# Kernel optimization log

Hardware: AMD Instinct MI355X
Metric: run time of the kernel (lower is better)

The kernel has to match this reference:

```python
import jax, jax.numpy as jnp
import numpy as np

B, L, D = 32, 256, 512
D_STATE, D_CONV, EXPAND, NODE_DIM, D_FF = 16, 4, 2, 16, 2048
D_INNER = EXPAND * D
DT_RANK = D // 16


def _layernorm(x, g, b, eps=1e-5):
    mu = x.mean(-1, keepdims=True)
    var = ((x - mu) ** 2).mean(-1, keepdims=True)
    return (x - mu) * jax.lax.rsqrt(var + eps) * g + b


def _mamba(x, in_w, conv_w, conv_b, xproj_w, dt_w, dt_b, A_log, Dp, out_w):
    # Standard selective-scan (S6) Mamba inner block.
    Bb, Ll, _ = x.shape
    u, z = jnp.split(x @ in_w, 2, axis=-1)                # (B,L,d_inner) each
    pad = jnp.pad(u, ((0, 0), (D_CONV - 1, 0), (0, 0)))   # causal depthwise conv1d
    u = sum(pad[:, k:k + Ll, :] * conv_w[:, k] for k in range(D_CONV)) + conv_b
    u = jax.nn.silu(u)
    proj = u @ xproj_w                                    # (B,L,dt_rank+2*d_state)
    dt, Bm, Cm = jnp.split(proj, [DT_RANK, DT_RANK + D_STATE], axis=-1)
    dt = jax.nn.softplus(dt @ dt_w + dt_b)                # (B,L,d_inner)
    A = -jnp.exp(A_log)                                   # (d_inner,d_state)
    dA = jnp.exp(dt[..., None] * A)                       # (B,L,d_inner,d_state)
    dBu = dt[..., None] * Bm[:, :, None, :] * u[..., None]

    def step(h, inp):
        dA_t, dBu_t, C_t = inp
        h = dA_t * h + dBu_t
        return h, jnp.einsum('bds,bs->bd', h, C_t)

    h0 = jnp.zeros((Bb, D_INNER, D_STATE), x.dtype)
    _, ys = jax.lax.scan(step, h0, (dA.transpose(1, 0, 2, 3),
                                    dBu.transpose(1, 0, 2, 3),
                                    Cm.transpose(1, 0, 2)))
    y = ys.transpose(1, 0, 2) + u * Dp                    # (B,L,d_inner)
    return (y * jax.nn.silu(z)) @ out_w


def _forward(x,
             d_in_w, d_conv_w, d_conv_b, d_xproj_w, d_dt_w, d_dt_b, d_A_log, d_D, d_out_w, d_ln_g, d_ln_b,
             s_emb1, s_emb2, s_in_w, s_conv_w, s_conv_b, s_xproj_w, s_dt_w, s_dt_b, s_A_log, s_D, s_out_w, s_ln_g, s_ln_b,
             f_ln_g, f_ln_b, f_w1, f_b1, f_w2, f_b2):
    # DiffSSM: selective SSM on the first-differenced sequence, residual + LN
    xd = jnp.concatenate([x[:, :1], x[:, 1:] - x[:, :-1]], axis=1)
    x = _layernorm(x + _mamba(xd, d_in_w, d_conv_w, d_conv_b, d_xproj_w,
                              d_dt_w, d_dt_b, d_A_log, d_D, d_out_w),
                   d_ln_g, d_ln_b)
    # SpatialGraphMamba: learned adjacency over enc_in tokens, graph mix, SSM
    adj = jax.nn.softmax(jax.nn.relu(s_emb1 @ s_emb2.T), axis=-1)  # (enc_in,enc_in)
    xg = jnp.einsum('nl,bld->bnd', adj, x)
    x = _layernorm(x + _mamba(xg, s_in_w, s_conv_w, s_conv_b, s_xproj_w,
                              s_dt_w, s_dt_b, s_A_log, s_D, s_out_w),
                   s_ln_g, s_ln_b)
    # Pre-norm FFN with residual
    h = _layernorm(x, f_ln_g, f_ln_b)
    x = x + jax.nn.gelu(h @ f_w1 + f_b1) @ f_w2 + f_b2
    return x, adj


def setup_inputs() -> dict:
    key = jax.random.key(0)
    ks = iter(jax.random.split(key, 64))

    def rn(shape, s=0.02):
        return jax.random.normal(next(ks), shape, jnp.float32) * s

    A_log_init = jnp.log(jnp.broadcast_to(
        jnp.arange(1, D_STATE + 1, dtype=jnp.float32), (D_INNER, D_STATE)))
    dt_b_init = jnp.full((D_INNER,), -4.6, jnp.float32)  # softplus^-1(~0.01)

    inp = {'x': jax.random.normal(next(ks), (B, L, D), jnp.float32)}
    for p in ('d_', 's_'):
        inp[p + 'in_w'] = rn((D, 2 * D_INNER))
        inp[p + 'conv_w'] = rn((D_INNER, D_CONV), 0.1)
        inp[p + 'conv_b'] = jnp.zeros((D_INNER,), jnp.float32)
        inp[p + 'xproj_w'] = rn((D_INNER, DT_RANK + 2 * D_STATE))
        inp[p + 'dt_w'] = rn((DT_RANK, D_INNER))
        inp[p + 'dt_b'] = dt_b_init
        inp[p + 'A_log'] = A_log_init
        inp[p + 'D'] = jnp.ones((D_INNER,), jnp.float32)
        inp[p + 'out_w'] = rn((D_INNER, D))
        inp[p + 'ln_g'] = jnp.ones((D,), jnp.float32)
        inp[p + 'ln_b'] = jnp.zeros((D,), jnp.float32)
    inp['s_emb1'] = rn((L, NODE_DIM), 0.1)
    inp['s_emb2'] = rn((L, NODE_DIM), 0.1)
    inp['f_ln_g'] = jnp.ones((D,), jnp.float32)
    inp['f_ln_b'] = jnp.zeros((D,), jnp.float32)
    inp['f_w1'] = rn((D, D_FF))
    inp['f_b1'] = jnp.zeros((D_FF,), jnp.float32)
    inp['f_w2'] = rn((D_FF, D))
    inp['f_b2'] = jnp.zeros((D,), jnp.float32)
    return inp


def reference(x,
              d_in_w, d_conv_w, d_conv_b, d_xproj_w, d_dt_w, d_dt_b, d_A_log, d_D, d_out_w, d_ln_g, d_ln_b,
              s_emb1, s_emb2, s_in_w, s_conv_w, s_conv_b, s_xproj_w, s_dt_w, s_dt_b, s_A_log, s_D, s_out_w, s_ln_g, s_ln_b,
              f_ln_g, f_ln_b, f_w1, f_b1, f_w2, f_b2):
    return _forward(x,
                    d_in_w, d_conv_w, d_conv_b, d_xproj_w, d_dt_w, d_dt_b, d_A_log, d_D, d_out_w, d_ln_g, d_ln_b,
                    s_emb1, s_emb2, s_in_w, s_conv_w, s_conv_b, s_xproj_w, s_dt_w, s_dt_b, s_A_log, s_D, s_out_w, s_ln_g, s_ln_b,
                    f_ln_g, f_ln_b, f_w1, f_b1, f_w2, f_b2)
```

## Files before the change

kernel.cpp:

```cpp
#include <hip/hip_runtime.h>

#define DEV __device__ __forceinline__

typedef __bf16 bf16x8 __attribute__((ext_vector_type(8)));
typedef float  f32x4  __attribute__((ext_vector_type(4)));

DEV unsigned short f2b(float f) {
    union { float f; unsigned u; } v; v.f = f;
    unsigned r = v.u + 0x7fffu + ((v.u >> 16) & 1u);
    return (unsigned short)(r >> 16);
}
DEV float b2f(unsigned short h) {
    union { unsigned u; float f; } v; v.u = ((unsigned)h) << 16;
    return v.f;
}
DEV float sigmoidf_(float x) { return 1.f / (1.f + __expf(-x)); }
DEV float geluf_(float x) {
    float t = 0.7978845608028654f * (x + 0.044715f * x * x * x);
    return 0.5f * x * (1.f + tanhf(t));
}
DEV float softplusf_(float x) { return x > 15.f ? x : log1pf(__expf(x)); }
DEV void gload_lds16(const void* g, void* l) {
    __builtin_amdgcn_global_load_lds((const __attribute__((address_space(1))) void*)g,
                                     (__attribute__((address_space(3))) void*)l, 16, 0, 0);
}


struct WtDesc { const float* s; unsigned short* d; int K; int N; int t0; };
struct WtArgs { WtDesc m[12]; };

__global__ __launch_bounds__(256) void wtrans_k(WtArgs a) {
    __shared__ float tile[32][33];
    int t = blockIdx.x;
    int mi = 0;
#pragma unroll
    for (int j = 1; j < 12; j++) if (t >= a.m[j].t0) mi = j;
    const float* src0 = a.m[mi].s;
    unsigned short* dst0 = a.m[mi].d;
    const int K = a.m[mi].K, N = a.m[mi].N;
    const int lt = t - a.m[mi].t0;
    const int ntk = K >> 5;
    const int kt = lt % ntk, nt = lt / ntk;
    const int c = threadIdx.x & 31, r = threadIdx.x >> 5;
    const float* src = src0 + (size_t)(kt * 32) * N + nt * 32;
#pragma unroll
    for (int i = 0; i < 4; i++) tile[r + i * 8][c] = src[(size_t)(r + i * 8) * N + c];
    __syncthreads();
    unsigned short* dst = dst0 + (size_t)(nt * 32) * K + kt * 32;
#pragma unroll
    for (int i = 0; i < 4; i++) dst[(size_t)(r + i * 8) * K + c] = f2b(tile[c][r + i * 8]);
}

__global__ __launch_bounds__(256) void diff_k(const float* __restrict__ x,
                                              unsigned short* __restrict__ xd) {
    size_t i4 = (size_t)blockIdx.x * 256 + threadIdx.x;
    size_t idx = i4 * 4;
    int l = (int)((idx >> 9) & 255);
    float4 v = *(const float4*)&x[idx];
    if (l > 0) {
        float4 p = *(const float4*)&x[idx - 512];
        v.x -= p.x; v.y -= p.y; v.z -= p.z; v.w -= p.w;
    }
    unsigned short o[4] = {f2b(v.x), f2b(v.y), f2b(v.z), f2b(v.w)};
    *(unsigned long long*)&xd[idx] = *(unsigned long long*)o;
}

__global__ __launch_bounds__(256) void adj_k(const float* __restrict__ e1,
                                             const float* __restrict__ e2,
                                             float* __restrict__ adjf,
                                             unsigned short* __restrict__ adjb) {
    const int n = blockIdx.x, tid = threadIdx.x;
    __shared__ float e1s[16];
    __shared__ float redm[4], reds[4];
    if (tid < 16) e1s[tid] = e1[n * 16 + tid];
    __syncthreads();
    const float* e2r = e2 + tid * 16;
    float dot = 0.f;
#pragma unroll
    for (int k = 0; k < 16; k++) dot = fmaf(e1s[k], e2r[k], dot);
    float v = fmaxf(dot, 0.f);
    float m = v;
#pragma unroll
    for (int o = 32; o > 0; o >>= 1) m = fmaxf(m, __shfl_xor(m, o));
    const int lane = tid & 63, wv = tid >> 6;
    if (lane == 0) redm[wv] = m;
    __syncthreads();
    m = fmaxf(fmaxf(redm[0], redm[1]), fmaxf(redm[2], redm[3]));
    float e = __expf(v - m);
    float ssum = e;
#pragma unroll
    for (int o = 32; o > 0; o >>= 1) ssum += __shfl_xor(ssum, o);
    if (lane == 0) reds[wv] = ssum;
    __syncthreads();
    ssum = reds[0] + reds[1] + reds[2] + reds[3];
    float o = e / ssum;
    adjf[(size_t)n * 256 + tid] = o;
    adjb[(size_t)n * 256 + tid] = f2b(o);
}

template<int HBIAS, int HGELU>
__global__ __launch_bounds__(512, 2) void gemm256_k(
    const unsigned short* __restrict__ A, const unsigned short* __restrict__ Bt,
    unsigned short* __restrict__ C, const float* __restrict__ bias,
    int M, int N, int K, int lda) {
    constexpr int BM = 256, BN = 256, BK = 64;
    __shared__ __align__(16) unsigned short As[2][BM * BK];
    __shared__ __align__(16) unsigned short Bs[2][BN * BK];
    const int tid  = threadIdx.x;
    const int lane = tid & 63;
    const int wave = tid >> 6;
    const int wr = wave >> 2;
    const int wc = wave & 3;
    const int bm = blockIdx.x * BM, bn = blockIdx.y * BN;
    const int lrow  = lane & 15;
    const int klane = lane >> 4;

    f32x4 acc[8][4];
#pragma unroll
    for (int m = 0; m < 8; m++)
#pragma unroll
        for (int n = 0; n < 4; n++) {
            acc[m][n][0] = 0.f; acc[m][n][1] = 0.f; acc[m][n][2] = 0.f; acc[m][n][3] = 0.f;
        }

    auto STAGE = [&](int buf, int k0) {
#pragma unroll
        for (int it = 0; it < 4; ++it) {
            int flat = (it * 512 + tid) * 8;
            int r = flat >> 6, s = (flat & 63) >> 3;
            int c = (s ^ (r & 7)) * 8;
            gload_lds16(A + (size_t)(bm + r) * lda + (k0 + c),
                        &As[buf][(it * 512 + (tid & 448)) * 8]);
        }
#pragma unroll
        for (int it = 0; it < 4; ++it) {
            int flat = (it * 512 + tid) * 8;
            int r = flat >> 6, s = (flat & 63) >> 3;
            int c = (s ^ (r & 7)) * 8;
            gload_lds16(Bt + (size_t)(bn + r) * K + (k0 + c),
                        &Bs[buf][(it * 512 + (tid & 448)) * 8]);
        }
    };
    auto COMPUTE = [&](int buf) {
#pragma unroll
        for (int kk = 0; kk < 2; kk++) {
            bf16x8 af[8], bfv[4];
#pragma unroll
            for (int m = 0; m < 8; m++) {
                int rr = wr * 128 + m * 16 + lrow;
                int sl = (kk * 4 + klane) ^ (rr & 7);
                af[m] = *(const bf16x8*)&As[buf][rr * BK + sl * 8];
            }
#pragma unroll
            for (int n = 0; n < 4; n++) {
                int rr = wc * 64 + n * 16 + lrow;
                int sl = (kk * 4 + klane) ^ (rr & 7);
                bfv[n] = *(const bf16x8*)&Bs[buf][rr * BK + sl * 8];
            }
#pragma unroll
            for (int m = 0; m < 8; m++)
#pragma unroll
                for (int n = 0; n < 4; n++)
                    acc[m][n] = __builtin_amdgcn_mfma_f32_16x16x32_bf16(af[m], bfv[n], acc[m][n], 0, 0, 0);
        }
    };

    const int nt = K / BK;
    STAGE(0, 0);
    __syncthreads();
    for (int t = 0; t < nt; t += 2) {
        if (t + 1 < nt) STAGE(1, (t + 1) * BK);
        COMPUTE(0);
        __syncthreads();
        if (t + 1 < nt) {
            if (t + 2 < nt) STAGE(0, (t + 2) * BK);
            COMPUTE(1);
            if (t + 2 < nt) __syncthreads();
        }
    }

    const int r0 = (lane >> 4) << 2;
    unsigned short* Cs = As[0];
    constexpr int PITCH = BN + 8;
#pragma unroll
    for (int g = 0; g < 8; g++) {
        __syncthreads();
        if (wr == (g >> 2)) {
#pragma unroll
            for (int mm = 0; mm < 2; mm++) {
                const int m = (g & 3) * 2 + mm;
#pragma unroll
                for (int n = 0; n < 4; n++) {
                    const int cl = wc * 64 + n * 16 + lrow;
                    float bv = HBIAS ? bias[bn + cl] : 0.f;
#pragma unroll
                    for (int j = 0; j < 4; j++) {
                        float v = acc[m][n][j] + bv;
                        if (HGELU) v = geluf_(v);
                        Cs[(mm * 16 + r0 + j) * PITCH + cl] = f2b(v);
                    }
                }
            }
        }
        __syncthreads();
#pragma unroll
        for (int i = 0; i < 2; i++) {
            int flat = (i * 512 + tid) * 8;
            int row = flat >> 8, col = flat & 255;
            uint4 val = *(const uint4*)&Cs[row * PITCH + col];
            *(uint4*)&C[(size_t)(bm + g * 32 + row) * N + bn + col] = val;
        }
    }
}

template<int BM, int BN, int BK, int WRN, int FM, int FN,
         int OBF, int HBIAS, int HGELU, int HRES, int HSP>
__global__ __launch_bounds__(256) void gemm_k(
    const unsigned short* __restrict__ A, const unsigned short* __restrict__ Bt,
    void* __restrict__ C, const float* __restrict__ bias, const float* __restrict__ res,
    int M, int N, int K, int lda, long sA, long sB, long sC) {
    constexpr int SMASK = BK / 8 - 1;
    constexpr int KH    = BK / 32;
    __shared__ __align__(16) unsigned short As[BM * BK];
    __shared__ __align__(16) unsigned short Bs[BN * BK];
    const int tid  = threadIdx.x;
    const int lane = tid & 63;
    const int wave = tid >> 6;
    const int wr = wave / WRN, wc = wave % WRN;
    const int bm = blockIdx.x * BM, bn = blockIdx.y * BN;
    const unsigned short* Ab = A  + (size_t)blockIdx.z * sA;
    const unsigned short* Bb = Bt + (size_t)blockIdx.z * sB;
    const int lrow  = lane & 15;
    const int klane = lane >> 4;

    f32x4 acc[FM][FN];
#pragma unroll
    for (int m = 0; m < FM; m++)
#pragma unroll
        for (int n = 0; n < FN; n++) {
            acc[m][n][0] = 0.f; acc[m][n][1] = 0.f; acc[m][n][2] = 0.f; acc[m][n][3] = 0.f;
        }

    constexpr int AI = (BM * BK) / 2048;
    constexpr int BI = (BN * BK) / 2048;

    for (int k0 = 0; k0 < K; k0 += BK) {
#pragma unroll
        for (int it = 0; it < AI; ++it) {
            int flat = (it * 256 + tid) * 8;
            int r = flat / BK, s = (flat % BK) >> 3;
            int c = (s ^ (r & SMASK)) * 8;
            gload_lds16(Ab + (size_t)(bm + r) * lda + (k0 + c),
                        &As[(it * 256 + (tid & 192)) * 8]);
        }
#pragma unroll
        for (int it = 0; it < BI; ++it) {
            int flat = (it * 256 + tid) * 8;
            int r = flat / BK, s = (flat % BK) >> 3;
            int c = (s ^ (r & SMASK)) * 8;
            gload_lds16(Bb + (size_t)(bn + r) * K + (k0 + c),
                        &Bs[(it * 256 + (tid & 192)) * 8]);
        }
        __syncthreads();
#pragma unroll
        for (int kk = 0; kk < KH; kk++) {
            bf16x8 af[FM], bfv[FN];
#pragma unroll
            for (int m = 0; m < FM; m++) {
                int rr = wr * FM * 16 + m * 16 + lrow;
                int sl = (kk * 4 + klane) ^ (rr & SMASK);
                af[m] = *(const bf16x8*)&As[rr * BK + sl * 8];
            }
#pragma unroll
            for (int n = 0; n < FN; n++) {
                int rr = wc * FN * 16 + n * 16 + lrow;
                int sl = (kk * 4 + klane) ^ (rr & SMASK);
                bfv[n] = *(const bf16x8*)&Bs[rr * BK + sl * 8];
            }
#pragma unroll
            for (int m = 0; m < FM; m++)
#pragma unroll
                for (int n = 0; n < FN; n++)
                    acc[m][n] = __builtin_amdgcn_mfma_f32_16x16x32_bf16(af[m], bfv[n], acc[m][n], 0, 0, 0);
        }
        __syncthreads();
    }

    const int r0 = (lane >> 4) << 2;
    if (OBF) {
        unsigned short* Cs = Bs;
        constexpr int PITCH = BN + 8;
        unsigned short* Cg = (unsigned short*)C;
#pragma unroll
        for (int g = 0; g < BM / 32; g++) {
            __syncthreads();
            if (wr == (g * 2) / FM) {
                const int mb = (g * 2) % FM;
#pragma unroll
                for (int mm = 0; mm < 2; mm++) {
#pragma unroll
                    for (int n = 0; n < FN; n++) {
                        const int cl = wc * FN * 16 + n * 16 + lrow;
                        float bv = HBIAS ? bias[bn + cl] : 0.f;
#pragma unroll
                        for (int j = 0; j < 4; j++) {
                            float v = acc[mb + mm][n][j] + bv;
                            if (HSP)   v = softplusf_(v);
                            if (HGELU) v = geluf_(v);
                            Cs[(mm * 16 + r0 + j) * PITCH + cl] = f2b(v);
                        }
                    }
                }
            }
            __syncthreads();
#pragma unroll
            for (int i = 0; i < (32 * BN) / 2048; i++) {
                int flat = (i * 256 + tid) * 8;
                int row = flat / BN, col = flat % BN;
                uint4 val = *(const uint4*)&Cs[row * PITCH + col];
                size_t oi = (size_t)blockIdx.z * sC + (size_t)(bm + g * 32 + row) * N + bn + col;
                *(uint4*)&Cg[oi] = val;
            }
        }
    } else {
#pragma unroll
        for (int n = 0; n < FN; n++) {
            const int ccol = bn + wc * FN * 16 + n * 16 + lrow;
            float bv = HBIAS ? bias[ccol] : 0.f;
#pragma unroll
            for (int m = 0; m < FM; m++) {
#pragma unroll
                for (int j = 0; j < 4; j++) {
                    const int rrow = bm + wr * FM * 16 + m * 16 + r0 + j;
                    float v = acc[m][n][j] + bv;
                    if (HSP)   v = softplusf_(v);
                    if (HGELU) v = geluf_(v);
                    if (HRES)  v += res[(size_t)rrow * N + ccol];
                    ((float*)C)[(size_t)blockIdx.z * sC + (size_t)rrow * N + ccol] = v;
                }
            }
        }
    }
}

__global__ __launch_bounds__(256) void conv_k(const unsigned short* __restrict__ uz,
                                              const float* __restrict__ w,
                                              const float* __restrict__ cb,
                                              unsigned short* __restrict__ u) {
    int t = blockIdx.x * 256 + threadIdx.x;
    int dg = t & 127;
    size_t row = (size_t)(t >> 7);
    int l = (int)(row & 255);
    int d0 = dg * 8;
    float acc[8];
#pragma unroll
    for (int j = 0; j < 8; j++) acc[j] = cb[d0 + j];
#pragma unroll
    for (int k = 0; k < 4; k++) {
        int ls = l + k - 3;
        if (ls >= 0) {
            const unsigned short* src = uz + (((size_t)row + k - 3) << 11) + d0;
            uint4 v = *(const uint4*)src;
            const unsigned short* vs = (const unsigned short*)&v;
#pragma unroll
            for (int j = 0; j < 8; j++)
                acc[j] = fmaf(w[(d0 + j) * 4 + k], b2f(vs[j]), acc[j]);
        }
    }
    unsigned short o[8];
#pragma unroll
    for (int j = 0; j < 8; j++) {
        float a = acc[j];
        o[j] = f2b(a * sigmoidf_(a));
    }
    *(uint4*)(u + (row << 10) + d0) = *(const uint4*)o;
}

__global__ __launch_bounds__(256) void scan1_k(
    const float* __restrict__ dt,
    const unsigned short* __restrict__ u,
    const unsigned short* __restrict__ proj,
    const float* __restrict__ A_log,
    float* __restrict__ hend, float* __restrict__ Sc) {
    const int dg = blockIdx.x, c = blockIdx.y, b = blockIdx.z;
    const int d = dg * 256 + threadIdx.x;
    const size_t base = (size_t)b * 256 + c * 32;
    __shared__ float Bs[32][16];
    for (int i = threadIdx.x; i < 512; i += 256) {
        int r = i >> 4, s = i & 15;
        Bs[r][s] = b2f(proj[(base + r) * 64 + 32 + s]);
    }
    __syncthreads();
    float Aa[16];
#pragma unroll
    for (int s = 0; s < 16; s++) Aa[s] = -__expf(A_log[d * 16 + s]);
    float h[16];
#pragma unroll
    for (int s = 0; s < 16; s++) h[s] = 0.f;
    float ssum = 0.f;
    for (int l = 0; l < 32; l++) {
        size_t row = base + l;
        float dtv = dt[(row << 10) + d];
        float uu  = b2f(u[(row << 10) + d]);
        float du  = dtv * uu;
        ssum += dtv;
#pragma unroll
        for (int s = 0; s < 16; s++)
            h[s] = __expf(dtv * Aa[s]) * h[s] + du * Bs[l][s];
    }
    size_t o = (size_t)(b * 8 + c) * 1024 + d;
    Sc[o] = ssum;
#pragma unroll
    for (int s = 0; s < 16; s++) hend[o * 16 + s] = h[s];
}

__global__ __launch_bounds__(256) void scan2_k(
    const float* __restrict__ hend, const float* __restrict__ Sc,
    const float* __restrict__ A_log, float* __restrict__ hstart) {
    const int d = blockIdx.x * 256 + threadIdx.x;
    const int b = blockIdx.y;
    float Aa[16];
#pragma unroll
    for (int s = 0; s < 16; s++) Aa[s] = -__expf(A_log[d * 16 + s]);
    float h[16];
#pragma unroll
    for (int s = 0; s < 16; s++) h[s] = 0.f;
    for (int c = 0; c < 8; c++) {
        size_t o = (size_t)(b * 8 + c) * 1024 + d;
#pragma unroll
        for (int s = 0; s < 16; s++) hstart[o * 16 + s] = h[s];
        float sc = Sc[o];
#pragma unroll
        for (int s = 0; s < 16; s++)
            h[s] = __expf(sc * Aa[s]) * h[s] + hend[o * 16 + s];
    }
}

__global__ __launch_bounds__(256) void scan3_k(
    const float* __restrict__ dt,
    const unsigned short* __restrict__ u,
    const unsigned short* __restrict__ uz,
    const unsigned short* __restrict__ proj,
    const float* __restrict__ A_log,
    const float* __restrict__ Dp,
    const float* __restrict__ hstart,
    unsigned short* __restrict__ yg) {
    const int dg = blockIdx.x, c = blockIdx.y, b = blockIdx.z;
    const int d = dg * 256 + threadIdx.x;
    const size_t base = (size_t)b * 256 + c * 32;
    __shared__ float BCs[32][32];
    for (int i = threadIdx.x; i < 1024; i += 256) {
        int r = i >> 5, s = i & 31;
        BCs[r][s] = b2f(proj[(base + r) * 64 + 32 + s]);
    }
    __syncthreads();
    float Aa[16];
#pragma unroll
    for (int s = 0; s < 16; s++) Aa[s] = -__expf(A_log[d * 16 + s]);
    const float Dd = Dp[d];
    float h[16];
    size_t ho = ((size_t)(b * 8 + c) * 1024 + d) * 16;
#pragma unroll
    for (int s = 0; s < 16; s++) h[s] = hstart[ho + s];
    for (int l = 0; l < 32; l++) {
        size_t row = base + l;
        float dtv = dt[(row << 10) + d];
        float uu  = b2f(u[(row << 10) + d]);
        float zz  = b2f(uz[(row << 11) + 1024 + d]);
        float du  = dtv * uu;
        float y = 0.f;
#pragma unroll
        for (int s = 0; s < 16; s++) {
            h[s] = __expf(dtv * Aa[s]) * h[s] + du * BCs[l][s];
            y = fmaf(h[s], BCs[l][16 + s], y);
        }
        y = fmaf(uu, Dd, y);
        yg[(row << 10) + d] = f2b(y * (zz * sigmoidf_(zz)));
    }
}

template<int HRES, int OF32, int OBF>
__global__ __launch_bounds__(256) void ln_k(const float* __restrict__ xin,
                                            const float* __restrict__ resin,
                                            const float* __restrict__ g,
                                            const float* __restrict__ b,
                                            float* __restrict__ outf,
                                            unsigned short* __restrict__ outb) {
    const int row = blockIdx.x, tid = threadIdx.x;
    float2 v = ((const float2*)(xin + (size_t)row * 512))[tid];
    if (HRES) {
        float2 r2 = ((const float2*)(resin + (size_t)row * 512))[tid];
        v.x += r2.x; v.y += r2.y;
    }
    float s = v.x + v.y, q = v.x * v.x + v.y * v.y;
#pragma unroll
    for (int o = 32; o > 0; o >>= 1) { s += __shfl_xor(s, o); q += __shfl_xor(q, o); }
    __shared__ float sm[4], qm[4];
    const int lane = tid & 63, wv = tid >> 6;
    if (lane == 0) { sm[wv] = s; qm[wv] = q; }
    __syncthreads();
    s = sm[0] + sm[1] + sm[2] + sm[3];
    q = qm[0] + qm[1] + qm[2] + qm[3];
    const float mu = s * (1.f / 512.f);
    const float ri = rsqrtf(q * (1.f / 512.f) - mu * mu + 1e-5f);
    float2 gg = ((const float2*)g)[tid];
    float2 bb = ((const float2*)b)[tid];
    float o0 = (v.x - mu) * ri * gg.x + bb.x;
    float o1 = (v.y - mu) * ri * gg.y + bb.y;
    if (OF32) ((float2*)(outf + (size_t)row * 512))[tid] = make_float2(o0, o1);
    if (OBF) {
        unsigned short* ob = outb + (size_t)row * 512 + tid * 2;
        ob[0] = f2b(o0); ob[1] = f2b(o1);
    }
}

__global__ __launch_bounds__(256) void trans_k(const float* __restrict__ x1,
                                               unsigned short* __restrict__ xt) {
    __shared__ float tile[32][33];
    const int b = blockIdx.z;
    const int d0 = blockIdx.x * 32, l0 = blockIdx.y * 32;
    const int c = threadIdx.x & 31, r = threadIdx.x >> 5;
    const float* src = x1 + ((size_t)b * 256 + l0) * 512 + d0;
#pragma unroll
    for (int i = 0; i < 4; i++) tile[r + i * 8][c] = src[(size_t)(r + i * 8) * 512 + c];
    __syncthreads();
    unsigned short* dst = xt + ((size_t)b * 512 + d0) * 256 + l0;
#pragma unroll
    for (int i = 0; i < 4; i++) dst[(size_t)(r + i * 8) * 256 + c] = f2b(tile[c][r + i * 8]);
}

constexpr size_t OFF_WT_DIN  = 0;
constexpr size_t OFF_WT_SIN  = OFF_WT_DIN  + 2048ull * 512 * 2;
constexpr size_t OFF_WT_DOUT = OFF_WT_SIN  + 2048ull * 512 * 2;
constexpr size_t OFF_WT_SOUT = OFF_WT_DOUT + 512ull * 1024 * 2;
constexpr size_t OFF_WT_F1   = OFF_WT_SOUT + 512ull * 1024 * 2;
constexpr size_t OFF_WT_F2   = OFF_WT_F1   + 2048ull * 512 * 2;
constexpr size_t OFF_XPT_D   = OFF_WT_F2   + 512ull * 2048 * 2;
constexpr size_t OFF_XPT_S   = OFF_XPT_D   + 64ull * 1024 * 2;
constexpr size_t OFF_DTT_D   = OFF_XPT_S   + 64ull * 1024 * 2;
constexpr size_t OFF_DTT_S   = OFF_DTT_D   + 1024ull * 32 * 2;
constexpr size_t OFF_ACT     = OFF_DTT_S   + 1024ull * 32 * 2;
constexpr size_t OFF_UZ      = OFF_ACT  + 8192ull * 512 * 2;
constexpr size_t OFF_U       = OFF_UZ   + 8192ull * 2048 * 2;
constexpr size_t OFF_PROJ    = OFF_U    + 8192ull * 1024 * 2;
constexpr size_t OFF_YG      = OFF_PROJ + 8192ull * 64 * 2;
constexpr size_t OFF_MOUT    = OFF_YG   + 8192ull * 1024 * 2;
constexpr size_t OFF_X1      = OFF_MOUT + 8192ull * 512 * 4;
constexpr size_t OFF_X2      = OFF_X1   + 8192ull * 512 * 4;
constexpr size_t OFF_X1T     = OFF_X2   + 8192ull * 512 * 4;
constexpr size_t OFF_ADJB    = OFF_X1T  + 32ull * 512 * 256 * 2;
constexpr size_t OFF_DT      = OFF_ADJB + 256ull * 256 * 2;
constexpr size_t OFF_HST     = OFF_DT   + 8192ull * 1024 * 4;
constexpr size_t OFF_SC      = OFF_HST  + 32ull * 8 * 1024 * 16 * 4;

extern "C" void kernel_launch(void* const* d_in, const int* in_sizes, int n_in,
                              void* d_out, int out_size, void* d_ws, size_t ws_size,
                              hipStream_t stream) {
    (void)in_sizes; (void)n_in; (void)out_size; (void)ws_size;
    const float* x      = (const float*)d_in[0];
    const float* dinw   = (const float*)d_in[1];
    const float* dconvw = (const float*)d_in[2];
    const float* dconvb = (const float*)d_in[3];
    const float* dxproj = (const float*)d_in[4];
    const float* ddtw   = (const float*)d_in[5];
    const float* ddtb   = (const float*)d_in[6];
    const float* dAlog  = (const float*)d_in[7];
    const float* dD     = (const float*)d_in[8];
    const float* doutw  = (const float*)d_in[9];
    const float* dlng   = (const float*)d_in[10];
    const float* dlnb   = (const float*)d_in[11];
    const float* sinw   = (const float*)d_in[12];
    const float* sconvw = (const float*)d_in[13];
    const float* sconvb = (const float*)d_in[14];
    const float* sxproj = (const float*)d_in[15];
    const float* sdtw   = (const float*)d_in[16];
    const float* sdtb   = (const float*)d_in[17];
    const float* sAlog  = (const float*)d_in[18];
    const float* sD     = (const float*)d_in[19];
    const float* soutw  = (const float*)d_in[20];
    const float* slng   = (const float*)d_in[21];
    const float* slnb   = (const float*)d_in[22];
    const float* semb1  = (const float*)d_in[23];
    const float* semb2  = (const float*)d_in[24];
    const float* flng   = (const float*)d_in[25];
    const float* flnb   = (const float*)d_in[26];
    const float* fw1    = (const float*)d_in[27];
    const float* fb1    = (const float*)d_in[28];
    const float* fw2    = (const float*)d_in[29];
    const float* fb2    = (const float*)d_in[30];

    char* ws = (char*)d_ws;
    unsigned short* wtDin  = (unsigned short*)(ws + OFF_WT_DIN);
    unsigned short* wtSin  = (unsigned short*)(ws + OFF_WT_SIN);
    unsigned short* wtDout = (unsigned short*)(ws + OFF_WT_DOUT);
    unsigned short* wtSout = (unsigned short*)(ws + OFF_WT_SOUT);
    unsigned short* wtF1   = (unsigned short*)(ws + OFF_WT_F1);
    unsigned short* wtF2   = (unsigned short*)(ws + OFF_WT_F2);
    unsigned short* xptD   = (unsigned short*)(ws + OFF_XPT_D);
    unsigned short* xptS   = (unsigned short*)(ws + OFF_XPT_S);
    unsigned short* dttD   = (unsigned short*)(ws + OFF_DTT_D);
    unsigned short* dttS   = (unsigned short*)(ws + OFF_DTT_S);
    unsigned short* actIn  = (unsigned short*)(ws + OFF_ACT);
    unsigned short* uzBuf  = (unsigned short*)(ws + OFF_UZ);
    unsigned short* uBuf   = (unsigned short*)(ws + OFF_U);
    unsigned short* projB  = (unsigned short*)(ws + OFF_PROJ);
    unsigned short* ygBuf  = (unsigned short*)(ws + OFF_YG);
    float*          moutB  = (float*)(ws + OFF_MOUT);
    float*          hendB  = moutB;
    float*          x1Buf  = (float*)(ws + OFF_X1);
    float*          x2Buf  = (float*)(ws + OFF_X2);
    unsigned short* x1tBuf = (unsigned short*)(ws + OFF_X1T);
    unsigned short* adjB   = (unsigned short*)(ws + OFF_ADJB);
    float*          dtBuf  = (float*)(ws + OFF_DT);
    float*          hstB   = (float*)(ws + OFF_HST);
    float*          scB    = (float*)(ws + OFF_SC);
    unsigned short* hBuf   = uBuf;
    unsigned short* midBuf = uzBuf;

    float* outX   = (float*)d_out;
    float* outAdj = outX + 4194304;

    WtArgs wa;
    wa.m[0]  = WtDesc{dinw,   wtDin,  512,  2048, 0};
    wa.m[1]  = WtDesc{sinw,   wtSin,  512,  2048, 1024};
    wa.m[2]  = WtDesc{doutw,  wtDout, 1024, 512,  2048};
    wa.m[3]  = WtDesc{soutw,  wtSout, 1024, 512,  2560};
    wa.m[4]  = WtDesc{fw1,    wtF1,   512,  2048, 3072};
    wa.m[5]  = WtDesc{fw2,    wtF2,   2048, 512,  4096};
    wa.m[6]  = WtDesc{dxproj, xptD,   1024, 64,   5120};
    wa.m[7]  = WtDesc{sxproj, xptS,   1024, 64,   5184};
    wa.m[8]  = WtDesc{ddtw,   dttD,   32,   1024, 5248};
    wa.m[9]  = WtDesc{sdtw,   dttS,   32,   1024, 5280};
    wa.m[10] = WtDesc{dinw,   wtDin,  512,  2048, 0x7fffffff};
    wa.m[11] = WtDesc{dinw,   wtDin,  512,  2048, 0x7fffffff};
    wtrans_k<<<dim3(5312), dim3(256), 0, stream>>>(wa);

    diff_k<<<dim3(4096), dim3(256), 0, stream>>>(x, actIn);
    adj_k<<<dim3(256), dim3(256), 0, stream>>>(semb1, semb2, outAdj, adjB);

    gemm256_k<0,0><<<dim3(32,8), dim3(512), 0, stream>>>(
        actIn, wtDin, uzBuf, nullptr, 8192, 2048, 512, 512);
    conv_k<<<dim3(4096), dim3(256), 0, stream>>>(uzBuf, dconvw, dconvb, uBuf);
    gemm_k<64,64,64,2,2,2, 1,0,0,0,0><<<dim3(128,1,1), dim3(256), 0, stream>>>(
        uBuf, xptD, projB, nullptr, nullptr, 8192, 64, 1024, 1024, 0, 0, 0);
    gemm_k<128,128,32,2,4,4, 0,1,0,0,1><<<dim3(64,8,1), dim3(256), 0, stream>>>(
        projB, dttD, dtBuf, ddtb, nullptr, 8192, 1024, 32, 64, 0, 0, 0);
    scan1_k<<<dim3(4,8,32), dim3(256), 0, stream>>>(dtBuf, uBuf, projB, dAlog, hendB, scB);
    scan2_k<<<dim3(4,32),   dim3(256), 0, stream>>>(hendB, scB, dAlog, hstB);
    scan3_k<<<dim3(4,8,32), dim3(256), 0, stream>>>(dtBuf, uBuf, uzBuf, projB, dAlog, dD, hstB, ygBuf);
    gemm_k<128,128,64,2,4,4, 0,0,0,0,0><<<dim3(64,4,1), dim3(256), 0, stream>>>(
        ygBuf, wtDout, moutB, nullptr, nullptr, 8192, 512, 1024, 1024, 0, 0, 0);
    ln_k<1,1,0><<<dim3(8192), dim3(256), 0, stream>>>(moutB, x, dlng, dlnb, x1Buf, nullptr);

    trans_k<<<dim3(16,8,32), dim3(256), 0, stream>>>(x1Buf, x1tBuf);
    gemm_k<128,128,64,2,4,4, 1,0,0,0,0><<<dim3(2,4,32), dim3(256), 0, stream>>>(
        adjB, x1tBuf, actIn, nullptr, nullptr, 256, 512, 256, 256, 0, 131072, 131072);
    gemm256_k<0,0><<<dim3(32,8), dim3(512), 0, stream>>>(
        actIn, wtSin, uzBuf, nullptr, 8192, 2048, 512, 512);
    conv_k<<<dim3(4096), dim3(256), 0, stream>>>(uzBuf, sconvw, sconvb, uBuf);
    gemm_k<64,64,64,2,2,2, 1,0,0,0,0><<<dim3(128,1,1), dim3(256), 0, stream>>>(
        uBuf, xptS, projB, nullptr, nullptr, 8192, 64, 1024, 1024, 0, 0, 0);
    gemm_k<128,128,32,2,4,4, 0,1,0,0,1><<<dim3(64,8,1), dim3(256), 0, stream>>>(
        projB, dttS, dtBuf, sdtb, nullptr, 8192, 1024, 32, 64, 0, 0, 0);
    scan1_k<<<dim3(4,8,32), dim3(256), 0, stream>>>(dtBuf, uBuf, projB, sAlog, hendB, scB);
    scan2_k<<<dim3(4,32),   dim3(256), 0, stream>>>(hendB, scB, sAlog, hstB);
    scan3_k<<<dim3(4,8,32), dim3(256), 0, stream>>>(dtBuf, uBuf, uzBuf, projB, sAlog, sD, hstB, ygBuf);
    gemm_k<128,128,64,2,4,4, 0,0,0,0,0><<<dim3(64,4,1), dim3(256), 0, stream>>>(
        ygBuf, wtSout, moutB, nullptr, nullptr, 8192, 512, 1024, 1024, 0, 0, 0);
    ln_k<1,1,0><<<dim3(8192), dim3(256), 0, stream>>>(moutB, x1Buf, slng, slnb, x2Buf, nullptr);

    ln_k<0,0,1><<<dim3(8192), dim3(256), 0, stream>>>(x2Buf, nullptr, flng, flnb, nullptr, hBuf);
    gemm256_k<1,1><<<dim3(32,8), dim3(512), 0, stream>>>(
        hBuf, wtF1, midBuf, fb1, 8192, 2048, 512, 512);
    gemm_k<128,128,64,2,4,4, 0,1,0,1,0><<<dim3(64,4,1), dim3(256), 0, stream>>>(
        midBuf, wtF2, outX, fb2, x2Buf, 8192, 512, 2048, 2048, 0, 0, 0);
}
```

Before: 637.7 us.

## Restructure gemm256 main loop into phased MFMA schedule; store dt as bf16

The 256-tile GEMM main loop is split into four sub-phases per K tile. Each phase loads a quarter of the fragments, issues the next tile's async global-to-LDS prefetch in phase 0, and brackets its MFMAs with s_setprio and raw s_barrier, using an explicit vmcnt wait only at the end of the tile. Separately, the dt projection now writes bf16 instead of fp32 and both scan kernels read bf16, halving dt traffic. The bf16 dt costs precision in the softplus output that feeds exp in the scan, and the hand-written barrier and waitcnt scheme depends on correct ordering of LDS reuse.

Result: slower. 697.6 us (+9.4%).

```diff
diff --git a/kernel.cpp b/kernel.cpp
--- a/kernel.cpp
+++ b/kernel.cpp
@@ -23,6 +23,9 @@
 DEV void gload_lds16(const void* g, void* l) {
     __builtin_amdgcn_global_load_lds((const __attribute__((address_space(1))) void*)g,
                                      (__attribute__((address_space(3))) void*)l, 16, 0, 0);
+}
+template<int N> DEV void waitv() {
+    asm volatile("s_waitcnt vmcnt(%0)" :: "n"(N) : "memory");
 }
 
 
@@ -141,41 +144,52 @@
                         &Bs[buf][(it * 512 + (tid & 448)) * 8]);
         }
     };
-    auto COMPUTE = [&](int buf) {
-#pragma unroll
-        for (int kk = 0; kk < 2; kk++) {
-            bf16x8 af[8], bfv[4];
-#pragma unroll
-            for (int m = 0; m < 8; m++) {
-                int rr = wr * 128 + m * 16 + lrow;
-                int sl = (kk * 4 + klane) ^ (rr & 7);
-                af[m] = *(const bf16x8*)&As[buf][rr * BK + sl * 8];
-            }
-#pragma unroll
-            for (int n = 0; n < 4; n++) {
-                int rr = wc * 64 + n * 16 + lrow;
-                int sl = (kk * 4 + klane) ^ (rr & 7);
-                bfv[n] = *(const bf16x8*)&Bs[buf][rr * BK + sl * 8];
-            }
-#pragma unroll
-            for (int m = 0; m < 8; m++)
-#pragma unroll
-                for (int n = 0; n < 4; n++)
-                    acc[m][n] = __builtin_amdgcn_mfma_f32_16x16x32_bf16(af[m], bfv[n], acc[m][n], 0, 0, 0);
-        }
-    };
 
     const int nt = K / BK;
     STAGE(0, 0);
-    __syncthreads();
-    for (int t = 0; t < nt; t += 2) {
-        if (t + 1 < nt) STAGE(1, (t + 1) * BK);
-        COMPUTE(0);
-        __syncthreads();
-        if (t + 1 < nt) {
-            if (t + 2 < nt) STAGE(0, (t + 2) * BK);
-            COMPUTE(1);
-            if (t + 2 < nt) __syncthreads();
+    waitv<0>();
+    __syncthreads();
+
+    for (int t = 0; t < nt; ++t) {
+        const int b = t & 1;
+#pragma unroll
+        for (int ph = 0; ph < 4; ++ph) {
+            const int mh = ph >> 1, nh = ph & 1;
+            bf16x8 af[2][4], bfv[2][2];
+#pragma unroll
+            for (int kk = 0; kk < 2; kk++) {
+#pragma unroll
+                for (int m = 0; m < 4; m++) {
+                    int rr = wr * 128 + (mh * 4 + m) * 16 + lrow;
+                    int sl = (kk * 4 + klane) ^ (rr & 7);
+                    af[kk][m] = *(const bf16x8*)&As[b][rr * BK + sl * 8];
+                }
+#pragma unroll
+                for (int n = 0; n < 2; n++) {
+                    int rr = wc * 64 + (nh * 2 + n) * 16 + lrow;
+                    int sl = (kk * 4 + klane) ^ (rr & 7);
+                    bfv[kk][n] = *(const bf16x8*)&Bs[b][rr * BK + sl * 8];
+                }
+            }
+            if (ph == 0 && t + 1 < nt) STAGE(b ^ 1, (t + 1) * BK);
+            __builtin_amdgcn_s_barrier();
+            __builtin_amdgcn_s_setprio(1);
+#pragma unroll
+            for (int kk = 0; kk < 2; kk++)
+#pragma unroll
+                for (int m = 0; m < 4; m++)
+#pragma unroll
+                    for (int n = 0; n < 2; n++)
+                        acc[mh * 4 + m][nh * 2 + n] = __builtin_amdgcn_mfma_f32_16x16x32_bf16(
+                            af[kk][m], bfv[kk][n], acc[mh * 4 + m][nh * 2 + n], 0, 0, 0);
+            __builtin_amdgcn_s_setprio(0);
+            if (ph == 3) {
+                if (t + 1 < nt) waitv<0>();
+                __builtin_amdgcn_s_barrier();
+                __builtin_amdgcn_sched_barrier(0);
+            } else {
+                __builtin_amdgcn_s_barrier();
+            }
         }
     }
 
@@ -377,7 +391,7 @@
 }
 
 __global__ __launch_bounds__(256) void scan1_k(
-    const float* __restrict__ dt,
+    const unsigned short* __restrict__ dt,
     const unsigned short* __restrict__ u,
     const unsigned short* __restrict__ proj,
     const float* __restrict__ A_log,
@@ -400,7 +414,7 @@
     float ssum = 0.f;
     for (int l = 0; l < 32; l++) {
         size_t row = base + l;
-        float dtv = dt[(row << 10) + d];
+        float dtv = b2f(dt[(row << 10) + d]);
         float uu  = b2f(u[(row << 10) + d]);
         float du  = dtv * uu;
         ssum += dtv;
@@ -437,7 +451,7 @@
 }
 
 __global__ __launch_bounds__(256) void scan3_k(
-    const float* __restrict__ dt,
+    const unsigned short* __restrict__ dt,
     const unsigned short* __restrict__ u,
     const unsigned short* __restrict__ uz,
     const unsigned short* __restrict__ proj,
@@ -464,7 +478,7 @@
     for (int s = 0; s < 16; s++) h[s] = hstart[ho + s];
     for (int l = 0; l < 32; l++) {
         size_t row = base + l;
-        float dtv = dt[(row << 10) + d];
+        float dtv = b2f(dt[(row << 10) + d]);
         float uu  = b2f(u[(row << 10) + d]);
         float zz  = b2f(uz[(row << 11) + 1024 + d]);
         float du  = dtv * uu;
@@ -550,7 +564,7 @@
 constexpr size_t OFF_X1T     = OFF_X2   + 8192ull * 512 * 4;
 constexpr size_t OFF_ADJB    = OFF_X1T  + 32ull * 512 * 256 * 2;
 constexpr size_t OFF_DT      = OFF_ADJB + 256ull * 256 * 2;
-constexpr size_t OFF_HST     = OFF_DT   + 8192ull * 1024 * 4;
+constexpr size_t OFF_HST     = OFF_DT   + 8192ull * 1024 * 2;
 constexpr size_t OFF_SC      = OFF_HST  + 32ull * 8 * 1024 * 16 * 4;
 
 extern "C" void kernel_launch(void* const* d_in, const int* in_sizes, int n_in,
@@ -611,7 +625,7 @@
     float*          x2Buf  = (float*)(ws + OFF_X2);
     unsigned short* x1tBuf = (unsigned short*)(ws + OFF_X1T);
     unsigned short* adjB   = (unsigned short*)(ws + OFF_ADJB);
-    float*          dtBuf  = (float*)(ws + OFF_DT);
+    unsigned short* dtBuf  = (unsigned short*)(ws + OFF_DT);
     float*          hstB   = (float*)(ws + OFF_HST);
     float*          scB    = (float*)(ws + OFF_SC);
     unsigned short* hBuf   = uBuf;
@@ -643,7 +657,7 @@
     conv_k<<<dim3(4096), dim3(256), 0, stream>>>(uzBuf, dconvw, dconvb, uBuf);
     gemm_k<64,64,64,2,2,2, 1,0,0,0,0><<<dim3(128,1,1), dim3(256), 0, stream>>>(
         uBuf, xptD, projB, nullptr, nullptr, 8192, 64, 1024, 1024, 0, 0, 0);
-    gemm_k<128,128,32,2,4,4, 0,1,0,0,1><<<dim3(64,8,1), dim3(256), 0, stream>>>(
+    gemm_k<128,128,32,2,4,4, 1,1,0,0,1><<<dim3(64,8,1), dim3(256), 0, stream>>>(
         projB, dttD, dtBuf, ddtb, nullptr, 8192, 1024, 32, 64, 0, 0, 0);
     scan1_k<<<dim3(4,8,32), dim3(256), 0, stream>>>(dtBuf, uBuf, projB, dAlog, hendB, scB);
     scan2_k<<<dim3(4,32),   dim3(256), 0, stream>>>(hendB, scB, dAlog, hstB);
@@ -660,7 +674,7 @@
     conv_k<<<dim3(4096), dim3(256), 0, stream>>>(uzBuf, sconvw, sconvb, uBuf);
     gemm_k<64,64,64,2,2,2, 1,0,0,0,0><<<dim3(128,1,1), dim3(256), 0, stream>>>(
         uBuf, xptS, projB, nullptr, nullptr, 8192, 64, 1024, 1024, 0, 0, 0);
-    gemm_k<128,128,32,2,4,4, 0,1,0,0,1><<<dim3(64,8,1), dim3(256), 0, stream>>>(
+    gemm_k<128,128,32,2,4,4, 1,1,0,0,1><<<dim3(64,8,1), dim3(256), 0, stream>>>(
         projB, dttS, dtBuf, sdtb, nullptr, 8192, 1024, 32, 64, 0, 0, 0);
     scan1_k<<<dim3(4,8,32), dim3(256), 0, stream>>>(dtBuf, uBuf, projB, sAlog, hendB, scB);
     scan2_k<<<dim3(4,32),   dim3(256), 0, stream>>>(hendB, scB, sAlog, hstB);
```
